# Optimization experiments

Measured on AMD Instinct MI355X. Metric: run time of the kernel, lower is better.

The kernel has to match this reference:

```python
import jax, jax.numpy as jnp
import numpy as np
from jax import lax

V, E, H = 32000, 256, 512
B, S, T = 32, 512, 30
BOS = 1


def gru_cell(x, h, w_ih, w_hh, b_ih, b_hh):
    # PyTorch GRU cell math. x: [B,E_in], h: [B,H]
    gi = x @ w_ih.T + b_ih            # [B,3H]
    gh = h @ w_hh.T + b_hh            # [B,3H]
    i_r, i_z, i_n = jnp.split(gi, 3, axis=-1)
    h_r, h_z, h_n = jnp.split(gh, 3, axis=-1)
    r = jax.nn.sigmoid(i_r + h_r)
    z = jax.nn.sigmoid(i_z + h_z)
    n = jnp.tanh(i_n + r * h_n)
    return (1.0 - z) * n + z * h


def setup_inputs() -> dict:
    key = jax.random.key(0)
    ks = jax.random.split(key, 18)
    f = lambda k, shape: (jax.random.normal(k, shape, jnp.float32) * 0.05)
    return {
        "body": jax.random.randint(ks[0], (B, S), 0, V, dtype=jnp.int32),
        "max_new_tokens": T,
        "enc_emb": f(ks[1], (V, E)),
        "enc_wih_f": f(ks[2], (3 * H, E)),
        "enc_whh_f": f(ks[3], (3 * H, H)),
        "enc_bih_f": f(ks[4], (3 * H,)),
        "enc_bhh_f": f(ks[5], (3 * H,)),
        "enc_wih_b": f(ks[6], (3 * H, E)),
        "enc_whh_b": f(ks[7], (3 * H, H)),
        "enc_bih_b": f(ks[8], (3 * H,)),
        "enc_bhh_b": f(ks[9], (3 * H,)),
        "dec_emb": f(ks[10], (V, E)),
        "dec_wih": f(ks[11], (3 * H, E)),
        "dec_whh": f(ks[12], (3 * H, H)),
        "dec_bih": f(ks[13], (3 * H,)),
        "dec_bhh": f(ks[14], (3 * H,)),
        "fc_w": f(ks[15], (V, H)),
        "fc_b": f(ks[16], (V,)),
    }


def reference(body, max_new_tokens, enc_emb, enc_wih_f, enc_whh_f, enc_bih_f,
              enc_bhh_f, enc_wih_b, enc_whh_b, enc_bih_b, enc_bhh_b,
              dec_emb, dec_wih, dec_whh, dec_bih, dec_bhh, fc_w, fc_b):
    batch = body.shape[0]
    hdim = enc_whh_f.shape[1]

    # ----- Encoder: bidirectional GRU, sum of final fwd/bwd hidden states -----
    emb = enc_emb[body]                     # [B,S,E] (dropout = identity in eval)
    xs = jnp.swapaxes(emb, 0, 1)            # [S,B,E]
    h0 = jnp.zeros((batch, hdim), emb.dtype)

    def step_f(h, x):
        return gru_cell(x, h, enc_wih_f, enc_whh_f, enc_bih_f, enc_bhh_f), None

    def step_b(h, x):
        return gru_cell(x, h, enc_wih_b, enc_whh_b, enc_bih_b, enc_bhh_b), None

    h_fwd, _ = lax.scan(step_f, h0, xs)
    h_bwd, _ = lax.scan(step_b, h0, xs[::-1])
    hidden = h_fwd + h_bwd                  # [B,H]  (== hidden[0] + hidden[1])

    tok0 = jnp.full((batch,), BOS, dtype=jnp.int32)

    def dec_step(carry, _):
        h, tok = carry
        x = dec_emb[tok]                                    # [B,E]
        h = gru_cell(x, h, dec_wih, dec_whh, dec_bih, dec_bhh)
        logits = h @ fc_w.T + fc_b                          # [B,V]
        nxt = jnp.argmax(logits, axis=-1).astype(jnp.int32)
        return (h, nxt), logits

    _, logits_seq = lax.scan(dec_step, (hidden, tok0), None,
                             length=max_new_tokens)          # [T,B,V]
    return jnp.swapaxes(logits_seq, 0, 1)                    # [B,T,V]
```

## Files before the change

### kernel.cpp

```cpp
#include <hip/hip_runtime.h>
#include <math.h>

#define BB 32
#define SS 512
#define EE 256
#define HH 512
#define VV 32000
#define TT 30
#define WPH 516

typedef unsigned long long ull;

__device__ __forceinline__ float4 ldf4(const float* p) {
    return *reinterpret_cast<const float4*>(p);
}
__device__ __forceinline__ float sigmoidf_(float x) {
    return 1.0f / (1.0f + expf(-x));
}
__device__ __forceinline__ void fma4(float4& a, float s, const float4& b) {
    a.x = fmaf(s, b.x, a.x); a.y = fmaf(s, b.y, a.y);
    a.z = fmaf(s, b.z, a.z); a.w = fmaf(s, b.w, a.w);
}
__device__ __forceinline__ ull mkkey(float val, int v) {
    unsigned u = __float_as_uint(val);
    u = (u >> 31) ? ~u : (u | 0x80000000u);
    return ((ull)u << 32) | (0xFFFFFFFFu - (unsigned)v);
}
__device__ __forceinline__ ull sxmax(ull k, int m) {
    unsigned hi = (unsigned)(k >> 32), lo = (unsigned)k;
    unsigned oh = __shfl_xor(hi, m), ol = __shfl_xor(lo, m);
    ull o = ((ull)oh << 32) | ol;
    return o > k ? o : k;
}
__device__ __forceinline__ ull cld8(const ull* p) {
    return __hip_atomic_load(p, __ATOMIC_RELAXED, __HIP_MEMORY_SCOPE_AGENT);
}
__device__ __forceinline__ void cst4(float* p, float v) {
    __hip_atomic_store(p, v, __ATOMIC_RELAXED, __HIP_MEMORY_SCOPE_AGENT);
}

__device__ __forceinline__ void gbar(unsigned* fl, int me, int n, int tid,
                                     unsigned tgt) {
    __syncthreads();
    if (tid == 0)
        __hip_atomic_store(fl + (size_t)me * 32, tgt, __ATOMIC_RELEASE,
                           __HIP_MEMORY_SCOPE_AGENT);
    if (tid < n) {
        while (__hip_atomic_load(fl + (size_t)tid * 32, __ATOMIC_RELAXED,
                                 __HIP_MEMORY_SCOPE_AGENT) < tgt)
            __builtin_amdgcn_s_sleep(2);
    }
    __syncthreads();
}

#define GATE4(acc0, acc1, W, h00, h01, h10, h11, h20, h21, h30, h31) \
    fma4(acc0, W.x, h00); fma4(acc1, W.x, h01);                      \
    fma4(acc0, W.y, h10); fma4(acc1, W.y, h11);                      \
    fma4(acc0, W.z, h20); fma4(acc1, W.z, h21);                      \
    fma4(acc0, W.w, h30); fma4(acc1, W.w, h31);

#define XR4(vv, m) { vv.x += __shfl_xor(vv.x, m); vv.y += __shfl_xor(vv.y, m); \
                     vv.z += __shfl_xor(vv.z, m); vv.w += __shfl_xor(vv.w, m); }

__global__ __launch_bounds__(256, 1) void enc_persist3(
    const int* __restrict__ body,
    const float* __restrict__ enc_emb,
    const float* __restrict__ wih_f, const float* __restrict__ whh_f,
    const float* __restrict__ bih_f, const float* __restrict__ bhh_f,
    const float* __restrict__ wih_b, const float* __restrict__ whh_b,
    const float* __restrict__ bih_b, const float* __restrict__ bhh_b,
    float* __restrict__ hD,
    unsigned* __restrict__ flagE)
{
    const int bid = blockIdx.x;
    const int tid = threadIdx.x;
    const int d   = bid & 7;
    const int m   = bid >> 3;
    const int dir = d >> 2;
    const int bg  = d & 3;
    const int jc  = m;

    const float* wih = dir ? wih_b : wih_f;
    const float* whh = dir ? whh_b : whh_f;
    const float* bih = dir ? bih_b : bih_f;
    const float* bhh = dir ? bhh_b : bhh_f;

    __shared__ float wlds[16 * 3 * WPH];
    __shared__ float hlds[512 * 8];
    __shared__ float xlds[256 * 8];
    __shared__ float part[2][16][33];
    __shared__ float blds[16][4];

    for (int idx = tid; idx < 48 * 128; idx += 256) {
        const int row = idx >> 7;
        const int q   = idx & 127;
        const int jl0 = row / 3, g = row - jl0 * 3;
        const int k   = q * 4;
        float4 v = ldf4(whh + (size_t)(g * HH + jc * 16 + jl0) * HH + k);
        float* dst = wlds + row * WPH + k;
        dst[0] = v.x; dst[1] = v.y; dst[2] = v.z; dst[3] = v.w;
    }
    if (tid < 16) {
        const int jg = jc * 16 + tid;
        blds[tid][0] = bih[jg] + bhh[jg];
        blds[tid][1] = bih[jg + HH] + bhh[jg + HH];
        blds[tid][2] = bih[jg + 2 * HH];
        blds[tid][3] = bhh[jg + 2 * HH];
    }

    const int ks   = tid >> 4;
    const int jl   = tid & 15;
    const int jg   = jc * 16 + jl;
    const int lane = tid & 63;
    const int wv   = tid >> 6;
    const float* wj = wlds + (jl * 3) * WPH;
    const float* wr_i = wih + (size_t)jg            * EE;
    const float* wz_i = wih + (size_t)(jg + HH)     * EE;
    const float* wn_i = wih + (size_t)(jg + 2 * HH) * EE;
    float* hdom = hD + (size_t)d * 2 * 4096;
    unsigned* fdom = flagE + (size_t)d * 1024;

    for (int t = 0; t < SS; ++t) {
        const int p = t & 1;

        {
            const ull* hsU = (const ull*)(hdom + p * 4096);
            ull hv[8];
            #pragma unroll
            for (int i = 0; i < 8; ++i) hv[i] = cld8(hsU + tid * 8 + i);
            ull* hlU = (ull*)hlds;
            #pragma unroll
            for (int i = 0; i < 8; ++i) hlU[tid * 8 + i] = hv[i];
        }
        {
            const int sb = tid & 7, kc = tid >> 3;
            const int s = dir ? (SS - 1 - t) : t;
            const int tk = body[(bg * 8 + sb) * SS + s];
            const float* xr = enc_emb + (size_t)tk * EE + kc * 8;
            float4 v0 = ldf4(xr), v1 = ldf4(xr + 4);
            const int k0 = kc * 8;
            xlds[(k0 + 0) * 8 + sb] = v0.x; xlds[(k0 + 1) * 8 + sb] = v0.y;
            xlds[(k0 + 2) * 8 + sb] = v0.z; xlds[(k0 + 3) * 8 + sb] = v0.w;
            xlds[(k0 + 4) * 8 + sb] = v1.x; xlds[(k0 + 5) * 8 + sb] = v1.y;
            xlds[(k0 + 6) * 8 + sb] = v1.z; xlds[(k0 + 7) * 8 + sb] = v1.w;
        }
        __syncthreads();

        float4 aR0 = {0,0,0,0}, aR1 = {0,0,0,0};
        float4 aZ0 = {0,0,0,0}, aZ1 = {0,0,0,0};
        float4 aN0 = {0,0,0,0}, aN1 = {0,0,0,0};
        float4 aI0 = {0,0,0,0}, aI1 = {0,0,0,0};

        #pragma unroll
        for (int q = 0; q < 8; ++q) {
            const int k = ks * 32 + q * 4;
            float4 wr = ldf4(wj + 0 * WPH + k);
            float4 wz = ldf4(wj + 1 * WPH + k);
            float4 wn = ldf4(wj + 2 * WPH + k);
            const float* hk = hlds + k * 8;
            float4 h00 = ldf4(hk +  0), h01 = ldf4(hk +  4);
            float4 h10 = ldf4(hk +  8), h11 = ldf4(hk + 12);
            float4 h20 = ldf4(hk + 16), h21 = ldf4(hk + 20);
            float4 h30 = ldf4(hk + 24), h31 = ldf4(hk + 28);
            GATE4(aR0, aR1, wr, h00, h01, h10, h11, h20, h21, h30, h31);
            GATE4(aZ0, aZ1, wz, h00, h01, h10, h11, h20, h21, h30, h31);
            GATE4(aN0, aN1, wn, h00, h01, h10, h11, h20, h21, h30, h31);
        }
        #pragma unroll
        for (int q = 0; q < 4; ++q) {
            const int k = ks * 16 + q * 4;
            float4 wr = ldf4(wr_i + k);
            float4 wz = ldf4(wz_i + k);
            float4 wn = ldf4(wn_i + k);
            const float* xk = xlds + k * 8;
            float4 x00 = ldf4(xk +  0), x01 = ldf4(xk +  4);
            float4 x10 = ldf4(xk +  8), x11 = ldf4(xk + 12);
            float4 x20 = ldf4(xk + 16), x21 = ldf4(xk + 20);
            float4 x30 = ldf4(xk + 24), x31 = ldf4(xk + 28);
            GATE4(aR0, aR1, wr, x00, x01, x10, x11, x20, x21, x30, x31);
            GATE4(aZ0, aZ1, wz, x00, x01, x10, x11, x20, x21, x30, x31);
            GATE4(aI0, aI1, wn, x00, x01, x10, x11, x20, x21, x30, x31);
        }

        XR4(aR0, 16); XR4(aR0, 32); XR4(aR1, 16); XR4(aR1, 32);
        XR4(aZ0, 16); XR4(aZ0, 32); XR4(aZ1, 16); XR4(aZ1, 32);
        XR4(aN0, 16); XR4(aN0, 32); XR4(aN1, 16); XR4(aN1, 32);
        XR4(aI0, 16); XR4(aI0, 32); XR4(aI1, 16); XR4(aI1, 32);

        if (wv < 2 && (lane >> 4) == 0) {
            float* pr = &part[wv][jl][0];
            pr[ 0]=aR0.x; pr[ 1]=aR0.y; pr[ 2]=aR0.z; pr[ 3]=aR0.w;
            pr[ 4]=aR1.x; pr[ 5]=aR1.y; pr[ 6]=aR1.z; pr[ 7]=aR1.w;
            pr[ 8]=aZ0.x; pr[ 9]=aZ0.y; pr[10]=aZ0.z; pr[11]=aZ0.w;
            pr[12]=aZ1.x; pr[13]=aZ1.y; pr[14]=aZ1.z; pr[15]=aZ1.w;
            pr[16]=aN0.x; pr[17]=aN0.y; pr[18]=aN0.z; pr[19]=aN0.w;
            pr[20]=aN1.x; pr[21]=aN1.y; pr[22]=aN1.z; pr[23]=aN1.w;
            pr[24]=aI0.x; pr[25]=aI0.y; pr[26]=aI0.z; pr[27]=aI0.w;
            pr[28]=aI1.x; pr[29]=aI1.y; pr[30]=aI1.z; pr[31]=aI1.w;
        }
        __syncthreads();
        if (wv >= 2 && (lane >> 4) == 0) {
            float* pr = &part[wv - 2][jl][0];
            pr[ 0]+=aR0.x; pr[ 1]+=aR0.y; pr[ 2]+=aR0.z; pr[ 3]+=aR0.w;
            pr[ 4]+=aR1.x; pr[ 5]+=aR1.y; pr[ 6]+=aR1.z; pr[ 7]+=aR1.w;
            pr[ 8]+=aZ0.x; pr[ 9]+=aZ0.y; pr[10]+=aZ0.z; pr[11]+=aZ0.w;
            pr[12]+=aZ1.x; pr[13]+=aZ1.y; pr[14]+=aZ1.z; pr[15]+=aZ1.w;
            pr[16]+=aN0.x; pr[17]+=aN0.y; pr[18]+=aN0.z; pr[19]+=aN0.w;
            pr[20]+=aN1.x; pr[21]+=aN1.y; pr[22]+=aN1.z; pr[23]+=aN1.w;
            pr[24]+=aI0.x; pr[25]+=aI0.y; pr[26]+=aI0.z; pr[27]+=aI0.w;
            pr[28]+=aI1.x; pr[29]+=aI1.y; pr[30]+=aI1.z; pr[31]+=aI1.w;
        }
        __syncthreads();

        if (tid < 128) {
            const int j2 = tid >> 3, b = tid & 7;
            float sR = part[0][j2][b]      + part[1][j2][b]      + blds[j2][0];
            float sZ = part[0][j2][8 + b]  + part[1][j2][8 + b]  + blds[j2][1];
            float sN = part[0][j2][16 + b] + part[1][j2][16 + b] + blds[j2][3];
            float sI = part[0][j2][24 + b] + part[1][j2][24 + b] + blds[j2][2];
            const float r = sigmoidf_(sR);
            const float z = sigmoidf_(sZ);
            const float n = tanhf(sI + r * sN);
            const int jw = jc * 16 + j2;
            const float hold = hlds[jw * 8 + b];
            cst4(hdom + (p ^ 1) * 4096 + jw * 8 + b, (1.0f - z) * n + z * hold);
        }

        if (t < SS - 1)
            gbar(fdom, m, 32, tid, (unsigned)(t + 1));
        else
            __syncthreads();
    }
}

__global__ __launch_bounds__(256) void enc_fin(
    const float* __restrict__ hD, float* __restrict__ hdT)
{
    const int i = blockIdx.x * 256 + threadIdx.x;
    const int k = i >> 5, b = i & 31;
    const int bg = b >> 3, sb = b & 7;
    hdT[i] = hD[(size_t)bg * 8192 + k * 8 + sb]
           + hD[(size_t)(4 + bg) * 8192 + k * 8 + sb];
}

__global__ __launch_bounds__(1024, 4) void dec_persist3(
    const float* __restrict__ dec_emb,
    const float* __restrict__ wih, const float* __restrict__ whh,
    const float* __restrict__ bih, const float* __restrict__ bhh,
    const float* __restrict__ fc_w, const float* __restrict__ fc_b,
    const float* __restrict__ hdT,
    float* __restrict__ hdG,
    ull* __restrict__ cand,
    float* __restrict__ out,
    unsigned* __restrict__ flagD)
{
    const int bid = blockIdx.x;
    const int tid = threadIdx.x;

    __shared__ float hlds[512 * 32];
    __shared__ float xls[256 * 32];
    __shared__ float partD[16][64][4];
    __shared__ ull lwred[16][8][4];
    __shared__ ull candp[32][33];
    __shared__ int tokL[32];

    float bR = 0, bZ = 0, bI = 0, bN = 0;
    if (tid < 64) {
        const int j2 = bid * 2 + (tid & 1);
        bR = bih[j2] + bhh[j2];
        bZ = bih[j2 + HH] + bhh[j2 + HH];
        bI = bih[j2 + 2 * HH];
        bN = bhh[j2 + 2 * HH];
    }

    for (int i = tid; i < 4096; i += 1024) {
        *(float4*)(hlds + i * 4) = ldf4(hdT + i * 4);
    }

    for (int t = 0; t < TT; ++t) {
        if (t == 0) {
            if (tid < 32) tokL[tid] = 1;
        } else {
            {
                const int b = tid & 31, cc = tid >> 5;
                ull km = 0ull;
                #pragma unroll
                for (int i = 0; i < 8; ++i) {
                    ull k2 = cld8(cand + (size_t)(cc * 8 + i) * 32 + b);
                    if (k2 > km) km = k2;
                }
                candp[cc][b] = km;
            }
            __syncthreads();
            if (tid < 32) {
                ull m2 = candp[0][tid];
                for (int c2 = 1; c2 < 32; ++c2) {
                    ull k2 = candp[c2][tid];
                    if (k2 > m2) m2 = k2;
                }
                tokL[tid] = (int)(0xFFFFFFFFu - (unsigned)(m2 & 0xFFFFFFFFull));
            }
        }
        __syncthreads();

        {
            const int b = tid & 31, kc = tid >> 5;
            const float* xr = dec_emb + (size_t)tokL[b] * EE + kc * 8;
            float4 v0 = ldf4(xr), v1 = ldf4(xr + 4);
            const int k0 = kc * 8;
            xls[(k0 + 0) * 32 + b] = v0.x; xls[(k0 + 1) * 32 + b] = v0.y;
            xls[(k0 + 2) * 32 + b] = v0.z; xls[(k0 + 3) * 32 + b] = v0.w;
            xls[(k0 + 4) * 32 + b] = v1.x; xls[(k0 + 5) * 32 + b] = v1.y;
            xls[(k0 + 6) * 32 + b] = v1.z; xls[(k0 + 7) * 32 + b] = v1.w;
        }
        __syncthreads();

        {
            const int ks = tid >> 6, b = (tid >> 1) & 31, jl = tid & 1;
            const int j = bid * 2 + jl;
            float sR = 0.f, sZ = 0.f, sN = 0.f, sI = 0.f;
            const float* wr_h = whh + (size_t)j            * HH;
            const float* wz_h = whh + (size_t)(j + HH)     * HH;
            const float* wn_h = whh + (size_t)(j + 2 * HH) * HH;
            #pragma unroll
            for (int q = 0; q < 8; ++q) {
                const int k = ks * 32 + q * 4;
                float4 wr = ldf4(wr_h + k), wz = ldf4(wz_h + k), wn = ldf4(wn_h + k);
                float h0 = hlds[(k + 0) * 32 + b], h1 = hlds[(k + 1) * 32 + b];
                float h2 = hlds[(k + 2) * 32 + b], h3 = hlds[(k + 3) * 32 + b];
                sR = fmaf(wr.x, h0, fmaf(wr.y, h1, fmaf(wr.z, h2, fmaf(wr.w, h3, sR))));
                sZ = fmaf(wz.x, h0, fmaf(wz.y, h1, fmaf(wz.z, h2, fmaf(wz.w, h3, sZ))));
                sN = fmaf(wn.x, h0, fmaf(wn.y, h1, fmaf(wn.z, h2, fmaf(wn.w, h3, sN))));
            }
            const float* wr_x = wih + (size_t)j            * EE;
            const float* wz_x = wih + (size_t)(j + HH)     * EE;
            const float* wn_x = wih + (size_t)(j + 2 * HH) * EE;
            #pragma unroll
            for (int q = 0; q < 4; ++q) {
                const int k = ks * 16 + q * 4;
                float4 wr = ldf4(wr_x + k), wz = ldf4(wz_x + k), wn = ldf4(wn_x + k);
                float x0 = xls[(k + 0) * 32 + b], x1 = xls[(k + 1) * 32 + b];
                float x2 = xls[(k + 2) * 32 + b], x3 = xls[(k + 3) * 32 + b];
                sR = fmaf(wr.x, x0, fmaf(wr.y, x1, fmaf(wr.z, x2, fmaf(wr.w, x3, sR))));
                sZ = fmaf(wz.x, x0, fmaf(wz.y, x1, fmaf(wz.z, x2, fmaf(wz.w, x3, sZ))));
                sI = fmaf(wn.x, x0, fmaf(wn.y, x1, fmaf(wn.z, x2, fmaf(wn.w, x3, sI))));
            }
            float* pd = &partD[ks][b * 2 + jl][0];
            pd[0] = sR; pd[1] = sZ; pd[2] = sN; pd[3] = sI;
        }
        __syncthreads();
        if (tid < 64) {
            const int b = tid >> 1, jl = tid & 1;
            const int j = bid * 2 + jl;
            float sR = bR, sZ = bZ, sN = bN, sI = bI;
            #pragma unroll
            for (int q2 = 0; q2 < 16; ++q2) {
                sR += partD[q2][tid][0]; sZ += partD[q2][tid][1];
                sN += partD[q2][tid][2]; sI += partD[q2][tid][3];
            }
            const float r = sigmoidf_(sR);
            const float z = sigmoidf_(sZ);
            const float n = tanhf(sI + r * sN);
            const float hold = hlds[j * 32 + b];
            cst4(hdG + (size_t)j * 32 + b, (1.0f - z) * n + z * hold);
        }

        gbar(flagD, bid, 256, tid, (unsigned)(2 * t + 1));

        {
            const ull* hU = (const ull*)hdG;
            ull hv[8];
            #pragma unroll
            for (int i = 0; i < 8; ++i) hv[i] = cld8(hU + tid * 8 + i);
            ull* hlU = (ull*)hlds;
            #pragma unroll
            for (int i = 0; i < 8; ++i) hlU[tid * 8 + i] = hv[i];
        }
        __syncthreads();

        {
            const int wave = tid >> 6, lane = tid & 63;
            const int bh = lane & 7, ks = (lane >> 3) & 3, vh = lane >> 5;
            const int voff = wave * 8 + vh * 4;
            const int vb   = bid * 125;
            const int k0   = ks * 128;

            const int o0 = voff,     o1 = voff + 1;
            const int o2 = voff + 2, o3 = voff + 3;
            const int v0 = vb + (o0 < 125 ? o0 : 124);
            const int v1 = vb + (o1 < 125 ? o1 : 124);
            const int v2 = vb + (o2 < 125 ? o2 : 124);
            const int v3 = vb + (o3 < 125 ? o3 : 124);
            const float* w0p = fc_w + (size_t)v0 * HH;
            const float* w1p = fc_w + (size_t)v1 * HH;
            const float* w2p = fc_w + (size_t)v2 * HH;
            const float* w3p = fc_w + (size_t)v3 * HH;

            float4 acc0 = {0,0,0,0}, acc1 = {0,0,0,0};
            float4 acc2 = {0,0,0,0}, acc3 = {0,0,0,0};

            for (int kk = 0; kk < 128; kk += 4) {
                const int k = k0 + kk;
                float4 w0 = ldf4(w0p + k), w1 = ldf4(w1p + k);
                float4 w2 = ldf4(w2p + k), w3 = ldf4(w3p + k);
                const float* hb = hlds + k * 32 + bh * 4;
                float4 h0 = ldf4(hb), h1 = ldf4(hb + 32);
                float4 h2 = ldf4(hb + 64), h3 = ldf4(hb + 96);
                fma4(acc0, w0.x, h0); fma4(acc0, w0.y, h1); fma4(acc0, w0.z, h2); fma4(acc0, w0.w, h3);
                fma4(acc1, w1.x, h0); fma4(acc1, w1.y, h1); fma4(acc1, w1.z, h2); fma4(acc1, w1.w, h3);
                fma4(acc2, w2.x, h0); fma4(acc2, w2.y, h1); fma4(acc2, w2.z, h2); fma4(acc2, w2.w, h3);
                fma4(acc3, w3.x, h0); fma4(acc3, w3.y, h1); fma4(acc3, w3.z, h2); fma4(acc3, w3.w, h3);
            }
            XR4(acc0, 8); XR4(acc0, 16);
            XR4(acc1, 8); XR4(acc1, 16);
            XR4(acc2, 8); XR4(acc2, 16);
            XR4(acc3, 8); XR4(acc3, 16);

            const int b0 = bh * 4;
            ull kb0 = 0, kb1 = 0, kb2 = 0, kb3 = 0;
            #pragma unroll
            for (int i = 0; i < 4; ++i) {
                const int off = voff + i;
                if (off < 125) {
                    const int v = vb + off;
                    float4 a = (i == 0) ? acc0 : (i == 1) ? acc1
                             : (i == 2) ? acc2 : acc3;
                    const float fb = fc_b[v];
                    a.x += fb; a.y += fb; a.z += fb; a.w += fb;
                    if (ks == 0) {
                        out[((size_t)((b0 + 0) * TT + t)) * VV + v] = a.x;
                        out[((size_t)((b0 + 1) * TT + t)) * VV + v] = a.y;
                        out[((size_t)((b0 + 2) * TT + t)) * VV + v] = a.z;
                        out[((size_t)((b0 + 3) * TT + t)) * VV + v] = a.w;
                    }
                    ull t0 = mkkey(a.x, v); if (t0 > kb0) kb0 = t0;
                    ull t1 = mkkey(a.y, v); if (t1 > kb1) kb1 = t1;
                    ull t2 = mkkey(a.z, v); if (t2 > kb2) kb2 = t2;
                    ull t3 = mkkey(a.w, v); if (t3 > kb3) kb3 = t3;
                }
            }
            kb0 = sxmax(kb0, 32); kb1 = sxmax(kb1, 32);
            kb2 = sxmax(kb2, 32); kb3 = sxmax(kb3, 32);
            if (lane < 8) {
                lwred[wave][bh][0] = kb0; lwred[wave][bh][1] = kb1;
                lwred[wave][bh][2] = kb2; lwred[wave][bh][3] = kb3;
            }
        }
        __syncthreads();
        if (tid < 32) {
            ull km = lwred[0][tid >> 2][tid & 3];
            #pragma unroll
            for (int w2 = 1; w2 < 16; ++w2) {
                ull k2 = lwred[w2][tid >> 2][tid & 3];
                if (k2 > km) km = k2;
            }
            __hip_atomic_store(cand + (size_t)bid * 32 + tid, km,
                               __ATOMIC_RELAXED, __HIP_MEMORY_SCOPE_AGENT);
        }

        if (t < TT - 1)
            gbar(flagD, bid, 256, tid, (unsigned)(2 * t + 2));
    }
}

extern "C" void kernel_launch(void* const* d_in, const int* in_sizes, int n_in,
                              void* d_out, int out_size, void* d_ws, size_t ws_size,
                              hipStream_t stream) {
    (void)in_sizes; (void)n_in; (void)out_size; (void)ws_size;

    const int*   body    = (const int*)  d_in[0];
    const float* enc_emb = (const float*)d_in[2];
    const float* wih_f   = (const float*)d_in[3];
    const float* whh_f   = (const float*)d_in[4];
    const float* bih_f   = (const float*)d_in[5];
    const float* bhh_f   = (const float*)d_in[6];
    const float* wih_b   = (const float*)d_in[7];
    const float* whh_b   = (const float*)d_in[8];
    const float* bih_b   = (const float*)d_in[9];
    const float* bhh_b   = (const float*)d_in[10];
    const float* dec_emb = (const float*)d_in[11];
    const float* dwih    = (const float*)d_in[12];
    const float* dwhh    = (const float*)d_in[13];
    const float* dbih    = (const float*)d_in[14];
    const float* dbhh    = (const float*)d_in[15];
    const float* fc_w    = (const float*)d_in[16];
    const float* fc_b    = (const float*)d_in[17];
    float* out = (float*)d_out;

    char* ws = (char*)d_ws;
    float* hD    = (float*)(ws);
    float* hdT   = (float*)(ws + 262144);
    float* hdG   = (float*)(ws + 327680);
    ull*   cand  = (ull*)  (ws + 393216);
    unsigned* flagE = (unsigned*)(ws + 458752);
    unsigned* flagD = (unsigned*)(ws + 491520);

    (void)hipMemsetAsync(hD, 0, 262144, stream);
    (void)hipMemsetAsync(flagE, 0, 65536, stream);

    enc_persist3<<<256, 256, 0, stream>>>(
        body, enc_emb, wih_f, whh_f, bih_f, bhh_f,
        wih_b, whh_b, bih_b, bhh_b, hD, flagE);

    enc_fin<<<64, 256, 0, stream>>>(hD, hdT);

    dec_persist3<<<256, 1024, 0, stream>>>(
        dec_emb, dwih, dwhh, dbih, dbhh, fc_w, fc_b,
        hdT, hdG, cand, out, flagD);
}
```

Measured before the change: 6.290 ms.

## Re-tile encoder and decoder GRU/FC loops with padded LDS layouts

The encoder now gives each thread two hidden units across a finer K-split (8 units by 32 K-slices). It reduces across the full wave with shuffles, replacing the two-phase shared-memory partial sum. Hidden and input tiles in LDS get padded strides to avoid bank conflicts, and the decoder's FC stage computes 8 vocab rows per lane with an 8-way K split, reducing fully in-wave. The spin-wait sleep is shortened, and the final-step sync is dropped, trading more shuffle work and register pressure for fewer LDS passes and barriers.

```diff
diff --git a/kernel.cpp b/kernel.cpp
--- a/kernel.cpp
+++ b/kernel.cpp
@@ -26,17 +26,15 @@
     u = (u >> 31) ? ~u : (u | 0x80000000u);
     return ((ull)u << 32) | (0xFFFFFFFFu - (unsigned)v);
 }
-__device__ __forceinline__ ull sxmax(ull k, int m) {
-    unsigned hi = (unsigned)(k >> 32), lo = (unsigned)k;
-    unsigned oh = __shfl_xor(hi, m), ol = __shfl_xor(lo, m);
-    ull o = ((ull)oh << 32) | ol;
-    return o > k ? o : k;
-}
 __device__ __forceinline__ ull cld8(const ull* p) {
     return __hip_atomic_load(p, __ATOMIC_RELAXED, __HIP_MEMORY_SCOPE_AGENT);
 }
 __device__ __forceinline__ void cst4(float* p, float v) {
     __hip_atomic_store(p, v, __ATOMIC_RELAXED, __HIP_MEMORY_SCOPE_AGENT);
+}
+__device__ __forceinline__ void xr4(float4& v, int m) {
+    v.x += __shfl_xor(v.x, m); v.y += __shfl_xor(v.y, m);
+    v.z += __shfl_xor(v.z, m); v.w += __shfl_xor(v.w, m);
 }
 
 __device__ __forceinline__ void gbar(unsigned* fl, int me, int n, int tid,
@@ -48,7 +46,7 @@
     if (tid < n) {
         while (__hip_atomic_load(fl + (size_t)tid * 32, __ATOMIC_RELAXED,
                                  __HIP_MEMORY_SCOPE_AGENT) < tgt)
-            __builtin_amdgcn_s_sleep(2);
+            __builtin_amdgcn_s_sleep(1);
     }
     __syncthreads();
 }
@@ -59,10 +57,10 @@
     fma4(acc0, W.z, h20); fma4(acc1, W.z, h21);                      \
     fma4(acc0, W.w, h30); fma4(acc1, W.w, h31);
 
-#define XR4(vv, m) { vv.x += __shfl_xor(vv.x, m); vv.y += __shfl_xor(vv.y, m); \
-                     vv.z += __shfl_xor(vv.z, m); vv.w += __shfl_xor(vv.w, m); }
-
-__global__ __launch_bounds__(256, 1) void enc_persist3(
+#define HIDX(k) ((k) * 8 + (((k) >> 4) << 2))
+#define XIDX(k) ((k) * 8 + (((k) >> 3) << 2))
+
+__global__ __launch_bounds__(256, 1) void enc_persist4(
     const int* __restrict__ body,
     const float* __restrict__ enc_emb,
     const float* __restrict__ wih_f, const float* __restrict__ whh_f,
@@ -85,10 +83,10 @@
     const float* bih = dir ? bih_b : bih_f;
     const float* bhh = dir ? bhh_b : bhh_f;
 
-    __shared__ float wlds[16 * 3 * WPH];
-    __shared__ float hlds[512 * 8];
-    __shared__ float xlds[256 * 8];
-    __shared__ float part[2][16][33];
+    __shared__ float wlds[48 * WPH];
+    __shared__ float hlds[4224];
+    __shared__ float xlds[2176];
+    __shared__ float part[32 * 72];
     __shared__ float blds[16][4];
 
     for (int idx = tid; idx < 48 * 128; idx += 256) {
@@ -108,29 +106,23 @@
         blds[tid][3] = bhh[jg + 2 * HH];
     }
 
-    const int ks   = tid >> 4;
-    const int jl   = tid & 15;
-    const int jg   = jc * 16 + jl;
+    const int jl   = tid & 7;
+    const int ks   = tid >> 3;
     const int lane = tid & 63;
     const int wv   = tid >> 6;
-    const float* wj = wlds + (jl * 3) * WPH;
-    const float* wr_i = wih + (size_t)jg            * EE;
-    const float* wz_i = wih + (size_t)(jg + HH)     * EE;
-    const float* wn_i = wih + (size_t)(jg + 2 * HH) * EE;
+    const int j0   = jc * 16 + jl * 2;
+
     float* hdom = hD + (size_t)d * 2 * 4096;
     unsigned* fdom = flagE + (size_t)d * 1024;
 
     for (int t = 0; t < SS; ++t) {
         const int p = t & 1;
 
+        ull hv[8];
         {
             const ull* hsU = (const ull*)(hdom + p * 4096);
-            ull hv[8];
             #pragma unroll
             for (int i = 0; i < 8; ++i) hv[i] = cld8(hsU + tid * 8 + i);
-            ull* hlU = (ull*)hlds;
-            #pragma unroll
-            for (int i = 0; i < 8; ++i) hlU[tid * 8 + i] = hv[i];
         }
         {
             const int sb = tid & 7, kc = tid >> 3;
@@ -138,98 +130,113 @@
             const int tk = body[(bg * 8 + sb) * SS + s];
             const float* xr = enc_emb + (size_t)tk * EE + kc * 8;
             float4 v0 = ldf4(xr), v1 = ldf4(xr + 4);
-            const int k0 = kc * 8;
-            xlds[(k0 + 0) * 8 + sb] = v0.x; xlds[(k0 + 1) * 8 + sb] = v0.y;
-            xlds[(k0 + 2) * 8 + sb] = v0.z; xlds[(k0 + 3) * 8 + sb] = v0.w;
-            xlds[(k0 + 4) * 8 + sb] = v1.x; xlds[(k0 + 5) * 8 + sb] = v1.y;
-            xlds[(k0 + 6) * 8 + sb] = v1.z; xlds[(k0 + 7) * 8 + sb] = v1.w;
-        }
-        __syncthreads();
-
-        float4 aR0 = {0,0,0,0}, aR1 = {0,0,0,0};
-        float4 aZ0 = {0,0,0,0}, aZ1 = {0,0,0,0};
-        float4 aN0 = {0,0,0,0}, aN1 = {0,0,0,0};
-        float4 aI0 = {0,0,0,0}, aI1 = {0,0,0,0};
-
+            const int base = kc * 68;
+            xlds[base +  0 + sb] = v0.x; xlds[base +  8 + sb] = v0.y;
+            xlds[base + 16 + sb] = v0.z; xlds[base + 24 + sb] = v0.w;
+            xlds[base + 32 + sb] = v1.x; xlds[base + 40 + sb] = v1.y;
+            xlds[base + 48 + sb] = v1.z; xlds[base + 56 + sb] = v1.w;
+        }
+        {
+            ull* hlU = (ull*)hlds;
+            const int base = tid * 8 + (tid >> 3) * 2;
+            #pragma unroll
+            for (int i = 0; i < 8; ++i) hlU[base + i] = hv[i];
+        }
+        __syncthreads();
+
+        float4 acc[2][4][2];
         #pragma unroll
-        for (int q = 0; q < 8; ++q) {
-            const int k = ks * 32 + q * 4;
-            float4 wr = ldf4(wj + 0 * WPH + k);
-            float4 wz = ldf4(wj + 1 * WPH + k);
-            float4 wn = ldf4(wj + 2 * WPH + k);
-            const float* hk = hlds + k * 8;
-            float4 h00 = ldf4(hk +  0), h01 = ldf4(hk +  4);
-            float4 h10 = ldf4(hk +  8), h11 = ldf4(hk + 12);
-            float4 h20 = ldf4(hk + 16), h21 = ldf4(hk + 20);
-            float4 h30 = ldf4(hk + 24), h31 = ldf4(hk + 28);
-            GATE4(aR0, aR1, wr, h00, h01, h10, h11, h20, h21, h30, h31);
-            GATE4(aZ0, aZ1, wz, h00, h01, h10, h11, h20, h21, h30, h31);
-            GATE4(aN0, aN1, wn, h00, h01, h10, h11, h20, h21, h30, h31);
-        }
+        for (int jj = 0; jj < 2; ++jj)
+            #pragma unroll
+            for (int g = 0; g < 4; ++g)
+                #pragma unroll
+                for (int h2 = 0; h2 < 2; ++h2)
+                    acc[jj][g][h2] = make_float4(0.f, 0.f, 0.f, 0.f);
+
         #pragma unroll
         for (int q = 0; q < 4; ++q) {
             const int k = ks * 16 + q * 4;
-            float4 wr = ldf4(wr_i + k);
-            float4 wz = ldf4(wz_i + k);
-            float4 wn = ldf4(wn_i + k);
-            const float* xk = xlds + k * 8;
-            float4 x00 = ldf4(xk +  0), x01 = ldf4(xk +  4);
-            float4 x10 = ldf4(xk +  8), x11 = ldf4(xk + 12);
-            float4 x20 = ldf4(xk + 16), x21 = ldf4(xk + 20);
-            float4 x30 = ldf4(xk + 24), x31 = ldf4(xk + 28);
-            GATE4(aR0, aR1, wr, x00, x01, x10, x11, x20, x21, x30, x31);
-            GATE4(aZ0, aZ1, wz, x00, x01, x10, x11, x20, x21, x30, x31);
-            GATE4(aI0, aI1, wn, x00, x01, x10, x11, x20, x21, x30, x31);
-        }
-
-        XR4(aR0, 16); XR4(aR0, 32); XR4(aR1, 16); XR4(aR1, 32);
-        XR4(aZ0, 16); XR4(aZ0, 32); XR4(aZ1, 16); XR4(aZ1, 32);
-        XR4(aN0, 16); XR4(aN0, 32); XR4(aN1, 16); XR4(aN1, 32);
-        XR4(aI0, 16); XR4(aI0, 32); XR4(aI1, 16); XR4(aI1, 32);
-
-        if (wv < 2 && (lane >> 4) == 0) {
-            float* pr = &part[wv][jl][0];
-            pr[ 0]=aR0.x; pr[ 1]=aR0.y; pr[ 2]=aR0.z; pr[ 3]=aR0.w;
-            pr[ 4]=aR1.x; pr[ 5]=aR1.y; pr[ 6]=aR1.z; pr[ 7]=aR1.w;
-            pr[ 8]=aZ0.x; pr[ 9]=aZ0.y; pr[10]=aZ0.z; pr[11]=aZ0.w;
-            pr[12]=aZ1.x; pr[13]=aZ1.y; pr[14]=aZ1.z; pr[15]=aZ1.w;
-            pr[16]=aN0.x; pr[17]=aN0.y; pr[18]=aN0.z; pr[19]=aN0.w;
-            pr[20]=aN1.x; pr[21]=aN1.y; pr[22]=aN1.z; pr[23]=aN1.w;
-            pr[24]=aI0.x; pr[25]=aI0.y; pr[26]=aI0.z; pr[27]=aI0.w;
-            pr[28]=aI1.x; pr[29]=aI1.y; pr[30]=aI1.z; pr[31]=aI1.w;
-        }
-        __syncthreads();
-        if (wv >= 2 && (lane >> 4) == 0) {
-            float* pr = &part[wv - 2][jl][0];
-            pr[ 0]+=aR0.x; pr[ 1]+=aR0.y; pr[ 2]+=aR0.z; pr[ 3]+=aR0.w;
-            pr[ 4]+=aR1.x; pr[ 5]+=aR1.y; pr[ 6]+=aR1.z; pr[ 7]+=aR1.w;
-            pr[ 8]+=aZ0.x; pr[ 9]+=aZ0.y; pr[10]+=aZ0.z; pr[11]+=aZ0.w;
-            pr[12]+=aZ1.x; pr[13]+=aZ1.y; pr[14]+=aZ1.z; pr[15]+=aZ1.w;
-            pr[16]+=aN0.x; pr[17]+=aN0.y; pr[18]+=aN0.z; pr[19]+=aN0.w;
-            pr[20]+=aN1.x; pr[21]+=aN1.y; pr[22]+=aN1.z; pr[23]+=aN1.w;
-            pr[24]+=aI0.x; pr[25]+=aI0.y; pr[26]+=aI0.z; pr[27]+=aI0.w;
-            pr[28]+=aI1.x; pr[29]+=aI1.y; pr[30]+=aI1.z; pr[31]+=aI1.w;
+            const float* hk = hlds + k * 8 + ks * 4;
+            float4 h0 = ldf4(hk +  0), h1 = ldf4(hk +  4);
+            float4 h2 = ldf4(hk +  8), h3 = ldf4(hk + 12);
+            float4 h4 = ldf4(hk + 16), h5 = ldf4(hk + 20);
+            float4 h6 = ldf4(hk + 24), h7 = ldf4(hk + 28);
+            #pragma unroll
+            for (int jj = 0; jj < 2; ++jj) {
+                const float* wr = wlds + (size_t)((jl * 2 + jj) * 3) * WPH + k;
+                #pragma unroll
+                for (int g = 0; g < 3; ++g) {
+                    float4 W = ldf4(wr + g * WPH);
+                    GATE4(acc[jj][g][0], acc[jj][g][1], W,
+                          h0, h1, h2, h3, h4, h5, h6, h7);
+                }
+            }
+        }
+        #pragma unroll
+        for (int q = 0; q < 2; ++q) {
+            const int k = ks * 8 + q * 4;
+            const float* xk = xlds + k * 8 + ks * 4;
+            float4 x0 = ldf4(xk +  0), x1 = ldf4(xk +  4);
+            float4 x2 = ldf4(xk +  8), x3 = ldf4(xk + 12);
+            float4 x4 = ldf4(xk + 16), x5 = ldf4(xk + 20);
+            float4 x6 = ldf4(xk + 24), x7 = ldf4(xk + 28);
+            #pragma unroll
+            for (int jj = 0; jj < 2; ++jj) {
+                const int j = j0 + jj;
+                float4 Wr = ldf4(wih + (size_t)j            * EE + k);
+                float4 Wz = ldf4(wih + (size_t)(j + HH)     * EE + k);
+                float4 Wn = ldf4(wih + (size_t)(j + 2 * HH) * EE + k);
+                GATE4(acc[jj][0][0], acc[jj][0][1], Wr, x0,x1,x2,x3,x4,x5,x6,x7);
+                GATE4(acc[jj][1][0], acc[jj][1][1], Wz, x0,x1,x2,x3,x4,x5,x6,x7);
+                GATE4(acc[jj][3][0], acc[jj][3][1], Wn, x0,x1,x2,x3,x4,x5,x6,x7);
+            }
+        }
+
+        #pragma unroll
+        for (int jj = 0; jj < 2; ++jj)
+            #pragma unroll
+            for (int g = 0; g < 4; ++g)
+                #pragma unroll
+                for (int h2 = 0; h2 < 2; ++h2) {
+                    xr4(acc[jj][g][h2], 8);
+                    xr4(acc[jj][g][h2], 16);
+                    xr4(acc[jj][g][h2], 32);
+                }
+
+        if (lane < 8) {
+            float* pr = part + (size_t)(wv * 8 + lane) * 72;
+            #pragma unroll
+            for (int jj = 0; jj < 2; ++jj)
+                #pragma unroll
+                for (int g = 0; g < 4; ++g) {
+                    *(float4*)(pr + jj * 32 + g * 8)     = acc[jj][g][0];
+                    *(float4*)(pr + jj * 32 + g * 8 + 4) = acc[jj][g][1];
+                }
         }
         __syncthreads();
 
         if (tid < 128) {
             const int j2 = tid >> 3, b = tid & 7;
-            float sR = part[0][j2][b]      + part[1][j2][b]      + blds[j2][0];
-            float sZ = part[0][j2][8 + b]  + part[1][j2][8 + b]  + blds[j2][1];
-            float sN = part[0][j2][16 + b] + part[1][j2][16 + b] + blds[j2][3];
-            float sI = part[0][j2][24 + b] + part[1][j2][24 + b] + blds[j2][2];
+            const int jl2 = j2 >> 1, jj = j2 & 1;
+            const int off = jj * 32 + (b >> 2) * 4 + (b & 3);
+            float sR = 0.f, sZ = 0.f, sN = 0.f, sI = 0.f;
+            #pragma unroll
+            for (int w2 = 0; w2 < 4; ++w2) {
+                const float* pr = part + (size_t)(w2 * 8 + jl2) * 72 + off;
+                sR += pr[0]; sZ += pr[8]; sN += pr[16]; sI += pr[24];
+            }
+            sR += blds[j2][0]; sZ += blds[j2][1];
+            sI += blds[j2][2]; sN += blds[j2][3];
             const float r = sigmoidf_(sR);
             const float z = sigmoidf_(sZ);
             const float n = tanhf(sI + r * sN);
-            const int jw = jc * 16 + j2;
-            const float hold = hlds[jw * 8 + b];
-            cst4(hdom + (p ^ 1) * 4096 + jw * 8 + b, (1.0f - z) * n + z * hold);
+            const int jg = jc * 16 + j2;
+            const float hold = hlds[HIDX(jg) + b];
+            cst4(hdom + (p ^ 1) * 4096 + jg * 8 + b, (1.0f - z) * n + z * hold);
         }
 
         if (t < SS - 1)
             gbar(fdom, m, 32, tid, (unsigned)(t + 1));
-        else
-            __syncthreads();
     }
 }
 
@@ -243,7 +250,9 @@
            + hD[(size_t)(4 + bg) * 8192 + k * 8 + sb];
 }
 
-__global__ __launch_bounds__(1024, 4) void dec_persist3(
+#define HIDX2(k) ((k) * 32 + (((k) >> 6) << 2))
+
+__global__ __launch_bounds__(1024, 4) void dec_persist4(
     const float* __restrict__ dec_emb,
     const float* __restrict__ wih, const float* __restrict__ whh,
     const float* __restrict__ bih, const float* __restrict__ bhh,
@@ -257,7 +266,7 @@
     const int bid = blockIdx.x;
     const int tid = threadIdx.x;
 
-    __shared__ float hlds[512 * 32];
+    __shared__ float hlds2[16416];
     __shared__ float xls[256 * 32];
     __shared__ float partD[16][64][4];
     __shared__ ull lwred[16][8][4];
@@ -274,7 +283,7 @@
     }
 
     for (int i = tid; i < 4096; i += 1024) {
-        *(float4*)(hlds + i * 4) = ldf4(hdT + i * 4);
+        *(float4*)(hlds2 + i * 4 + ((i >> 9) << 2)) = ldf4(hdT + i * 4);
     }
 
     for (int t = 0; t < TT; ++t) {
@@ -319,6 +328,8 @@
             const int ks = tid >> 6, b = (tid >> 1) & 31, jl = tid & 1;
             const int j = bid * 2 + jl;
             float sR = 0.f, sZ = 0.f, sN = 0.f, sI = 0.f;
+            const float* hpA = hlds2 + (size_t)(ks * 32) * 32
+                             + ((ks >> 1) << 2) + b;
             const float* wr_h = whh + (size_t)j            * HH;
             const float* wz_h = whh + (size_t)(j + HH)     * HH;
             const float* wn_h = whh + (size_t)(j + 2 * HH) * HH;
@@ -326,8 +337,8 @@
             for (int q = 0; q < 8; ++q) {
                 const int k = ks * 32 + q * 4;
                 float4 wr = ldf4(wr_h + k), wz = ldf4(wz_h + k), wn = ldf4(wn_h + k);
-                float h0 = hlds[(k + 0) * 32 + b], h1 = hlds[(k + 1) * 32 + b];
-                float h2 = hlds[(k + 2) * 32 + b], h3 = hlds[(k + 3) * 32 + b];
+                const float* hq = hpA + q * 128;
+                float h0 = hq[0], h1 = hq[32], h2 = hq[64], h3 = hq[96];
                 sR = fmaf(wr.x, h0, fmaf(wr.y, h1, fmaf(wr.z, h2, fmaf(wr.w, h3, sR))));
                 sZ = fmaf(wz.x, h0, fmaf(wz.y, h1, fmaf(wz.z, h2, fmaf(wz.w, h3, sZ))));
                 sN = fmaf(wn.x, h0, fmaf(wn.y, h1, fmaf(wn.z, h2, fmaf(wn.w, h3, sN))));
@@ -361,7 +372,7 @@
             const float r = sigmoidf_(sR);
             const float z = sigmoidf_(sZ);
             const float n = tanhf(sI + r * sN);
-            const float hold = hlds[j * 32 + b];
+            const float hold = hlds2[HIDX2(j) + b];
             cst4(hdG + (size_t)j * 32 + b, (1.0f - z) * n + z * hold);
         }
 
@@ -372,78 +383,73 @@
             ull hv[8];
             #pragma unroll
             for (int i = 0; i < 8; ++i) hv[i] = cld8(hU + tid * 8 + i);
-            ull* hlU = (ull*)hlds;
-            #pragma unroll
-            for (int i = 0; i < 8; ++i) hlU[tid * 8 + i] = hv[i];
-        }
-        __syncthreads();
-
-        {
-            const int wave = tid >> 6, lane = tid & 63;
-            const int bh = lane & 7, ks = (lane >> 3) & 3, vh = lane >> 5;
-            const int voff = wave * 8 + vh * 4;
-            const int vb   = bid * 125;
-            const int k0   = ks * 128;
-
-            const int o0 = voff,     o1 = voff + 1;
-            const int o2 = voff + 2, o3 = voff + 3;
-            const int v0 = vb + (o0 < 125 ? o0 : 124);
-            const int v1 = vb + (o1 < 125 ? o1 : 124);
-            const int v2 = vb + (o2 < 125 ? o2 : 124);
-            const int v3 = vb + (o3 < 125 ? o3 : 124);
-            const float* w0p = fc_w + (size_t)v0 * HH;
-            const float* w1p = fc_w + (size_t)v1 * HH;
-            const float* w2p = fc_w + (size_t)v2 * HH;
-            const float* w3p = fc_w + (size_t)v3 * HH;
-
-            float4 acc0 = {0,0,0,0}, acc1 = {0,0,0,0};
-            float4 acc2 = {0,0,0,0}, acc3 = {0,0,0,0};
-
-            for (int kk = 0; kk < 128; kk += 4) {
+            const int k = tid >> 1, half = tid & 1;
+            ull* hlU = (ull*)hlds2;
+            const int base = k * 16 + ((k >> 6) << 1) + half * 8;
+            #pragma unroll
+            for (int i = 0; i < 8; ++i) hlU[base + i] = hv[i];
+        }
+        __syncthreads();
+
+        {
+            const int lane = tid & 63, wavei = tid >> 6;
+            const int bh = lane & 7, ksd = lane >> 3;
+            const int voff = wavei * 8;
+            const int vb = bid * 125;
+            const int k0 = ksd * 64;
+            const float* hB = hlds2 + (size_t)k0 * 32 + ksd * 4 + bh * 4;
+
+            const float* wp[8];
+            #pragma unroll
+            for (int i = 0; i < 8; ++i) {
+                int off = voff + i; if (off > 124) off = 124;
+                wp[i] = fc_w + (size_t)(vb + off) * HH;
+            }
+            float4 acc[8];
+            #pragma unroll
+            for (int i = 0; i < 8; ++i) acc[i] = make_float4(0.f, 0.f, 0.f, 0.f);
+
+            for (int kk = 0; kk < 64; kk += 4) {
                 const int k = k0 + kk;
-                float4 w0 = ldf4(w0p + k), w1 = ldf4(w1p + k);
-                float4 w2 = ldf4(w2p + k), w3 = ldf4(w3p + k);
-                const float* hb = hlds + k * 32 + bh * 4;
-                float4 h0 = ldf4(hb), h1 = ldf4(hb + 32);
-                float4 h2 = ldf4(hb + 64), h3 = ldf4(hb + 96);
-                fma4(acc0, w0.x, h0); fma4(acc0, w0.y, h1); fma4(acc0, w0.z, h2); fma4(acc0, w0.w, h3);
-                fma4(acc1, w1.x, h0); fma4(acc1, w1.y, h1); fma4(acc1, w1.z, h2); fma4(acc1, w1.w, h3);
-                fma4(acc2, w2.x, h0); fma4(acc2, w2.y, h1); fma4(acc2, w2.z, h2); fma4(acc2, w2.w, h3);
-                fma4(acc3, w3.x, h0); fma4(acc3, w3.y, h1); fma4(acc3, w3.z, h2); fma4(acc3, w3.w, h3);
-            }
-            XR4(acc0, 8); XR4(acc0, 16);
-            XR4(acc1, 8); XR4(acc1, 16);
-            XR4(acc2, 8); XR4(acc2, 16);
-            XR4(acc3, 8); XR4(acc3, 16);
-
-            const int b0 = bh * 4;
-            ull kb0 = 0, kb1 = 0, kb2 = 0, kb3 = 0;
-            #pragma unroll
-            for (int i = 0; i < 4; ++i) {
-                const int off = voff + i;
-                if (off < 125) {
-                    const int v = vb + off;
-                    float4 a = (i == 0) ? acc0 : (i == 1) ? acc1
-                             : (i == 2) ? acc2 : acc3;
-                    const float fb = fc_b[v];
-                    a.x += fb; a.y += fb; a.z += fb; a.w += fb;
-                    if (ks == 0) {
+                float4 wv4[8];
+                #pragma unroll
+                for (int i = 0; i < 8; ++i) wv4[i] = ldf4(wp[i] + k);
+                const float* hq = hB + kk * 32;
+                float4 h0 = ldf4(hq), h1 = ldf4(hq + 32);
+                float4 h2 = ldf4(hq + 64), h3 = ldf4(hq + 96);
+                #pragma unroll
+                for (int i = 0; i < 8; ++i) {
+                    fma4(acc[i], wv4[i].x, h0); fma4(acc[i], wv4[i].y, h1);
+                    fma4(acc[i], wv4[i].z, h2); fma4(acc[i], wv4[i].w, h3);
+                }
+            }
+            #pragma unroll
+            for (int i = 0; i < 8; ++i) {
+                xr4(acc[i], 8); xr4(acc[i], 16); xr4(acc[i], 32);
+            }
+            if (ksd == 0) {
+                ull kb0 = 0, kb1 = 0, kb2 = 0, kb3 = 0;
+                const int b0 = bh * 4;
+                #pragma unroll
+                for (int i = 0; i < 8; ++i) {
+                    const int off = voff + i;
+                    if (off < 125) {
+                        const int v = vb + off;
+                        const float fb = fc_b[v];
+                        float4 a = acc[i];
+                        a.x += fb; a.y += fb; a.z += fb; a.w += fb;
                         out[((size_t)((b0 + 0) * TT + t)) * VV + v] = a.x;
                         out[((size_t)((b0 + 1) * TT + t)) * VV + v] = a.y;
                         out[((size_t)((b0 + 2) * TT + t)) * VV + v] = a.z;
                         out[((size_t)((b0 + 3) * TT + t)) * VV + v] = a.w;
+                        ull t0 = mkkey(a.x, v); if (t0 > kb0) kb0 = t0;
+                        ull t1 = mkkey(a.y, v); if (t1 > kb1) kb1 = t1;
+                        ull t2 = mkkey(a.z, v); if (t2 > kb2) kb2 = t2;
+                        ull t3 = mkkey(a.w, v); if (t3 > kb3) kb3 = t3;
                     }
-                    ull t0 = mkkey(a.x, v); if (t0 > kb0) kb0 = t0;
-                    ull t1 = mkkey(a.y, v); if (t1 > kb1) kb1 = t1;
-                    ull t2 = mkkey(a.z, v); if (t2 > kb2) kb2 = t2;
-                    ull t3 = mkkey(a.w, v); if (t3 > kb3) kb3 = t3;
-                }
-            }
-            kb0 = sxmax(kb0, 32); kb1 = sxmax(kb1, 32);
-            kb2 = sxmax(kb2, 32); kb3 = sxmax(kb3, 32);
-            if (lane < 8) {
-                lwred[wave][bh][0] = kb0; lwred[wave][bh][1] = kb1;
-                lwred[wave][bh][2] = kb2; lwred[wave][bh][3] = kb3;
+                }
+                lwred[wavei][bh][0] = kb0; lwred[wavei][bh][1] = kb1;
+                lwred[wavei][bh][2] = kb2; lwred[wavei][bh][3] = kb3;
             }
         }
         __syncthreads();
@@ -498,13 +504,13 @@
     (void)hipMemsetAsync(hD, 0, 262144, stream);
     (void)hipMemsetAsync(flagE, 0, 65536, stream);
 
-    enc_persist3<<<256, 256, 0, stream>>>(
+    enc_persist4<<<256, 256, 0, stream>>>(
         body, enc_emb, wih_f, whh_f, bih_f, bhh_f,
         wih_b, whh_b, bih_b, bhh_b, hD, flagE);
 
     enc_fin<<<64, 256, 0, stream>>>(hD, hdT);
 
-    dec_persist3<<<256, 1024, 0, stream>>>(
+    dec_persist4<<<256, 1024, 0, stream>>>(
         dec_emb, dwih, dwhh, dbih, dbhh, fc_w, fc_b,
         hdT, hdG, cand, out, flagD);
 }
```

Result: slower. 8.060 ms (+28.1%).
